# Performance work log

Hardware: AMD Instinct MI355X
Metric: run time of the kernel (lower is better)

The kernel has to match this reference:

```python
import jax, jax.numpy as jnp
import numpy as np
from jax import lax

N, GH, GE, LH, LL = 19, 64, 64, 64, 2
B, T = 256, 256


def _normalized_adjacency(A):
    # A: (..., n, n). Add self-loops, symmetric degree normalization.
    n = A.shape[-1]
    A = A + jnp.eye(n, dtype=A.dtype)
    deg = jnp.clip(A.sum(axis=-1), 1e-6, None)  # (..., n)
    dis = deg ** -0.5
    return A * dis[..., :, None] * dis[..., None, :]


def _graph_encoder(A, w1_w, w1_b, w2_w, w2_b):
    # A: (B, T, n, n) -> (B, T, GE). Node features X = A rows.
    An = _normalized_adjacency(A)
    X = jax.nn.relu(An @ (A @ w1_w.T + w1_b))   # (B,T,n,GH)
    X = jax.nn.relu(An @ (X @ w2_w.T + w2_b))   # (B,T,n,GE)
    return X.mean(axis=-2)


def _lstm_layer(x, Wih, Whh, bih, bhh):
    # x: (B, T, D); PyTorch gate order i,f,g,o. Returns (B, T, H).
    Bb = x.shape[0]
    H = Whh.shape[1]
    xg = x @ Wih.T + (bih + bhh)  # precompute input contributions (B,T,4H)

    def step(carry, xt):
        h, c = carry
        gates = xt + h @ Whh.T
        i, f, g, o = jnp.split(gates, 4, axis=-1)
        c = jax.nn.sigmoid(f) * c + jax.nn.sigmoid(i) * jnp.tanh(g)
        h = jax.nn.sigmoid(o) * jnp.tanh(c)
        return (h, c), h

    h0 = jnp.zeros((Bb, H), x.dtype)
    (_, _), hs = lax.scan(step, (h0, h0), jnp.swapaxes(xg, 0, 1))
    return jnp.swapaxes(hs, 0, 1)


def setup_inputs() -> dict:
    key = jax.random.key(0)
    ks = jax.random.split(key, 20)
    s = 0.1
    inp = {
        'conn': jax.random.uniform(ks[0], (B, T, N, N), jnp.float32),
        'mask': jnp.ones((B, T), jnp.int32),
        'w1_w': jax.random.normal(ks[1], (GH, N), jnp.float32) * s,
        'w1_b': jax.random.normal(ks[2], (GH,), jnp.float32) * s,
        'w2_w': jax.random.normal(ks[3], (GE, GH), jnp.float32) * s,
        'w2_b': jax.random.normal(ks[4], (GE,), jnp.float32) * s,
        'lstm_Wih0': jax.random.normal(ks[5], (4 * LH, GE), jnp.float32) * s,
        'lstm_Whh0': jax.random.normal(ks[6], (4 * LH, LH), jnp.float32) * s,
        'lstm_bih0': jax.random.normal(ks[7], (4 * LH,), jnp.float32) * s,
        'lstm_bhh0': jax.random.normal(ks[8], (4 * LH,), jnp.float32) * s,
        'lstm_Wih1': jax.random.normal(ks[9], (4 * LH, LH), jnp.float32) * s,
        'lstm_Whh1': jax.random.normal(ks[10], (4 * LH, LH), jnp.float32) * s,
        'lstm_bih1': jax.random.normal(ks[11], (4 * LH,), jnp.float32) * s,
        'lstm_bhh1': jax.random.normal(ks[12], (4 * LH,), jnp.float32) * s,
        'fc1_w': jax.random.normal(ks[13], (32, LH), jnp.float32) * s,
        'fc1_b': jax.random.normal(ks[14], (32,), jnp.float32) * s,
        'fc2_w': jax.random.normal(ks[15], (2, 32), jnp.float32) * s,
        'fc2_b': jax.random.normal(ks[16], (2,), jnp.float32) * s,
    }
    return inp


def reference(conn, mask, w1_w, w1_b, w2_w, w2_b,
              lstm_Wih0, lstm_Whh0, lstm_bih0, lstm_bhh0,
              lstm_Wih1, lstm_Whh1, lstm_bih1, lstm_bhh1,
              fc1_w, fc1_b, fc2_w, fc2_b):
    emb = _graph_encoder(conn, w1_w, w1_b, w2_w, w2_b)  # (B,T,GE)
    mf = mask.astype(emb.dtype)
    emb = emb * mf[:, :, None]
    out = _lstm_layer(emb, lstm_Wih0, lstm_Whh0, lstm_bih0, lstm_bhh0)
    out = _lstm_layer(out, lstm_Wih1, lstm_Whh1, lstm_bih1, lstm_bhh1)  # (B,T,LH)
    lengths = jnp.clip(mask.sum(axis=1), 1, None)
    last_idx = jnp.clip(lengths - 1, 0, None)  # (B,)
    last_h = jnp.take_along_axis(out, last_idx[:, None, None], axis=1)[:, 0, :]
    h = jax.nn.relu(last_h @ fc1_w.T + fc1_b)
    return h @ fc2_w.T + fc2_b  # (B,2) logits
```

## Files before the change

kernel.cpp:

```cpp
#include <hip/hip_runtime.h>
#include <hip/hip_bf16.h>
#include <math.h>

#define GN 19
#define BB 256
#define TT 256

typedef short short8 __attribute__((ext_vector_type(8)));
typedef float f4 __attribute__((ext_vector_type(4)));

union Frag { int i[4]; short8 s; };

#define LWAIT() __asm__ volatile("s_waitcnt lgkmcnt(0)" ::: "memory")
#define WGBAR() __asm__ volatile("s_waitcnt lgkmcnt(0)\ns_barrier" ::: "memory")

__device__ __forceinline__ int pkbf(float a, float b) {
    __hip_bfloat162 h2 = __float22bfloat162_rn(make_float2(a, b));
    union { __hip_bfloat162 h; int i; } u; u.h = h2; return u.i;
}

__device__ __forceinline__ float rl(float v, int j) {
    return __int_as_float(__builtin_amdgcn_readlane(__float_as_int(v), j));
}
__device__ __forceinline__ float fexp2(float x) { return __builtin_amdgcn_exp2f(x); }
__device__ __forceinline__ float frcp(float x)  { return __builtin_amdgcn_rcpf(x); }
__device__ __forceinline__ float sigm(float x)  { return frcp(1.f + fexp2(-1.4426950408889634f * x)); }
__device__ __forceinline__ float tanha(float x) { float e = fexp2(2.8853900817779268f * x); return 1.f - 2.f * frcp(e + 1.f); }

__global__ __launch_bounds__(64) void encoder_mfma(
    const float* __restrict__ conn,
    const int*   __restrict__ mask,
    const float* __restrict__ w1_w,
    const float* __restrict__ w1_b,
    const float* __restrict__ w2_w,
    const float* __restrict__ w2_b,
    float* __restrict__ emb,
    int num_graphs)
{
    __shared__ float S[2304];
    __shared__ float dis[32];
    __shared__ float ps[256];

    const int t = threadIdx.x;
    const int l15 = t & 15;
    const int quad = t >> 4;

    float km[8];
    #pragma unroll
    for (int j = 0; j < 8; ++j) km[j] = (quad * 8 + j < GN) ? 1.f : 0.f;

    int rr[6], cc[6];
    #pragma unroll
    for (int i = 0; i < 6; ++i) {
        int e = t + 64 * i;
        rr[i] = e / GN;
        cc[i] = e - rr[i] * GN;
    }

    Frag w1F[4];
    #pragma unroll
    for (int nt = 0; nt < 4; ++nt) {
        int n = nt * 16 + l15;
        #pragma unroll
        for (int p = 0; p < 4; ++p) {
            int k0 = quad * 8 + 2 * p, k1 = k0 + 1;
            float a = (k0 < GN) ? w1_w[n * GN + k0] : 0.f;
            float b = (k1 < GN) ? w1_w[n * GN + k1] : 0.f;
            w1F[nt].i[p] = pkbf(a, b);
        }
    }
    Frag w2F[2][4];
    #pragma unroll
    for (int kt = 0; kt < 2; ++kt)
        #pragma unroll
        for (int nt = 0; nt < 4; ++nt) {
            int n = nt * 16 + l15;
            #pragma unroll
            for (int p = 0; p < 4; ++p) {
                int k = kt * 32 + quad * 8 + 2 * p;
                w2F[kt][nt].i[p] = pkbf(w2_w[n * 64 + k], w2_w[n * 64 + k + 1]);
            }
        }
    float b1v[4], b2v[4];
    #pragma unroll
    for (int nt = 0; nt < 4; ++nt) {
        b1v[nt] = w1_b[nt * 16 + l15];
        b2v[nt] = w2_b[nt * 16 + l15];
    }

    float pf[6];
    {
        int g0 = blockIdx.x < num_graphs ? blockIdx.x : 0;
        const float* Ag = conn + (size_t)g0 * (GN * GN);
        #pragma unroll
        for (int i = 0; i < 6; ++i) {
            int e = t + 64 * i;
            if (e < GN * GN) pf[i] = Ag[e];
        }
    }

    #pragma unroll 1
    for (int g = blockIdx.x; g < num_graphs; g += gridDim.x) {
        #pragma unroll
        for (int i = 0; i < 4; ++i) {
            int s = t + 64 * i;
            int row = s >> 3, c4 = s & 7;
            f4 z = {0.f, 0.f, 0.f, 0.f};
            *(f4*)&S[row * 68 + c4 * 4] = z;
        }
        LWAIT();
        #pragma unroll
        for (int i = 0; i < 6; ++i) {
            if (t + 64 * i < GN * GN) S[rr[i] * 68 + cc[i]] = pf[i];
        }
        {
            int gn = g + gridDim.x;
            const float* Ag = conn + (size_t)(gn < num_graphs ? gn : g) * (GN * GN);
            #pragma unroll
            for (int i = 0; i < 6; ++i) {
                int e = t + 64 * i;
                if (e < GN * GN) pf[i] = Ag[e];
            }
        }
        LWAIT();

        if (t < 32) {
            float dv = 0.f;
            if (t < GN) {
                float d = 1.0f;
                #pragma unroll
                for (int c4 = 0; c4 < 8; ++c4) {
                    f4 v = *(f4*)&S[t * 68 + c4 * 4];
                    d += v.x + v.y + v.z + v.w;
                }
                dv = rsqrtf(d);
            }
            dis[t] = dv;
        }
        LWAIT();

        float dk[8];
        {
            f4 v0 = *(f4*)&dis[quad * 8];
            f4 v1 = *(f4*)&dis[quad * 8 + 4];
            dk[0]=v0.x; dk[1]=v0.y; dk[2]=v0.z; dk[3]=v0.w;
            dk[4]=v1.x; dk[5]=v1.y; dk[6]=v1.z; dk[7]=v1.w;
        }
        Frag aF[2], anF[2];
        #pragma unroll
        for (int mt = 0; mt < 2; ++mt) {
            int m = l15 + 16 * mt;
            float dm = dis[m];
            f4 v0 = *(f4*)&S[m * 68 + quad * 8];
            f4 v1 = *(f4*)&S[m * 68 + quad * 8 + 4];
            float av[8] = {v0.x, v0.y, v0.z, v0.w, v1.x, v1.y, v1.z, v1.w};
            float an[8];
            #pragma unroll
            for (int j = 0; j < 8; ++j) {
                int k = quad * 8 + j;
                an[j] = (av[j] + (m == k ? 1.f : 0.f)) * dm * dk[j];
            }
            #pragma unroll
            for (int p = 0; p < 4; ++p) {
                aF[mt].i[p]  = pkbf(av[2*p], av[2*p+1]);
                anF[mt].i[p] = pkbf(an[2*p], an[2*p+1]);
            }
        }
        LWAIT();

        #pragma unroll
        for (int mt = 0; mt < 2; ++mt)
            #pragma unroll
            for (int nt = 0; nt < 4; ++nt) {
                float bb = b1v[nt];
                f4 c = {bb, bb, bb, bb};
                c = __builtin_amdgcn_mfma_f32_16x16x32_bf16(aF[mt].s, w1F[nt].s, c, 0, 0, 0);
                int col = nt * 16 + l15;
                #pragma unroll
                for (int r = 0; r < 4; ++r)
                    S[col * 36 + (mt * 16 + quad * 4 + r)] = c[r];
            }
        LWAIT();

        Frag hF[4];
        #pragma unroll
        for (int nt = 0; nt < 4; ++nt) {
            int n = nt * 16 + l15;
            f4 v0 = *(f4*)&S[n * 36 + quad * 8];
            f4 v1 = *(f4*)&S[n * 36 + quad * 8 + 4];
            float vv[8] = {v0.x, v0.y, v0.z, v0.w, v1.x, v1.y, v1.z, v1.w};
            #pragma unroll
            for (int p = 0; p < 4; ++p)
                hF[nt].i[p] = pkbf(vv[2*p] * km[2*p], vv[2*p+1] * km[2*p+1]);
        }
        LWAIT();

        #pragma unroll
        for (int mt = 0; mt < 2; ++mt)
            #pragma unroll
            for (int nt = 0; nt < 4; ++nt) {
                f4 c = {0.f, 0.f, 0.f, 0.f};
                c = __builtin_amdgcn_mfma_f32_16x16x32_bf16(anF[mt].s, hF[nt].s, c, 0, 0, 0);
                int col = nt * 16 + l15;
                #pragma unroll
                for (int r = 0; r < 4; ++r)
                    S[(mt * 16 + quad * 4 + r) * 68 + col] = fmaxf(c[r], 0.f);
            }
        LWAIT();

        Frag xF[2][2];
        #pragma unroll
        for (int mt = 0; mt < 2; ++mt) {
            int m = l15 + 16 * mt;
            #pragma unroll
            for (int kt = 0; kt < 2; ++kt) {
                f4 v0 = *(f4*)&S[m * 68 + kt * 32 + quad * 8];
                f4 v1 = *(f4*)&S[m * 68 + kt * 32 + quad * 8 + 4];
                xF[mt][kt].i[0] = pkbf(v0.x, v0.y);
                xF[mt][kt].i[1] = pkbf(v0.z, v0.w);
                xF[mt][kt].i[2] = pkbf(v1.x, v1.y);
                xF[mt][kt].i[3] = pkbf(v1.z, v1.w);
            }
        }
        LWAIT();

        #pragma unroll
        for (int mt = 0; mt < 2; ++mt)
            #pragma unroll
            for (int nt = 0; nt < 4; ++nt) {
                float bb = b2v[nt];
                f4 c = {bb, bb, bb, bb};
                c = __builtin_amdgcn_mfma_f32_16x16x32_bf16(xF[mt][0].s, w2F[0][nt].s, c, 0, 0, 0);
                c = __builtin_amdgcn_mfma_f32_16x16x32_bf16(xF[mt][1].s, w2F[1][nt].s, c, 0, 0, 0);
                int col = nt * 16 + l15;
                #pragma unroll
                for (int r = 0; r < 4; ++r)
                    S[col * 36 + (mt * 16 + quad * 4 + r)] = c[r];
            }
        LWAIT();

        #pragma unroll
        for (int nt = 0; nt < 4; ++nt) {
            int n = nt * 16 + l15;
            f4 v0 = *(f4*)&S[n * 36 + quad * 8];
            f4 v1 = *(f4*)&S[n * 36 + quad * 8 + 4];
            float vv[8] = {v0.x, v0.y, v0.z, v0.w, v1.x, v1.y, v1.z, v1.w};
            #pragma unroll
            for (int p = 0; p < 4; ++p)
                hF[nt].i[p] = pkbf(vv[2*p] * km[2*p], vv[2*p+1] * km[2*p+1]);
        }

        float cs[4];
        #pragma unroll
        for (int nt = 0; nt < 4; ++nt) cs[nt] = 0.f;
        #pragma unroll
        for (int mt = 0; mt < 2; ++mt)
            #pragma unroll
            for (int nt = 0; nt < 4; ++nt) {
                f4 c = {0.f, 0.f, 0.f, 0.f};
                c = __builtin_amdgcn_mfma_f32_16x16x32_bf16(anF[mt].s, hF[nt].s, c, 0, 0, 0);
                if (mt == 0) {
                    cs[nt] += fmaxf(c[0], 0.f) + fmaxf(c[1], 0.f)
                            + fmaxf(c[2], 0.f) + fmaxf(c[3], 0.f);
                } else if (quad == 0) {
                    cs[nt] += fmaxf(c[0], 0.f) + fmaxf(c[1], 0.f) + fmaxf(c[2], 0.f);
                }
            }
        #pragma unroll
        for (int nt = 0; nt < 4; ++nt)
            ps[quad * 64 + nt * 16 + l15] = cs[nt];
        LWAIT();
        float tot = ps[t] + ps[64 + t] + ps[128 + t] + ps[192 + t];
        float mf = (float)mask[g];
        emb[(size_t)g * 64 + t] = tot * (1.f / 19.f) * mf;
        LWAIT();
    }
}

__global__ __launch_bounds__(512, 2) void lstm_fused(
    const float* __restrict__ x,
    const int*   __restrict__ mask,
    const float* __restrict__ Wih0, const float* __restrict__ Whh0,
    const float* __restrict__ bih0, const float* __restrict__ bhh0,
    const float* __restrict__ Wih1, const float* __restrict__ Whh1,
    const float* __restrict__ bih1, const float* __restrict__ bhh1,
    const float* __restrict__ fc1_w, const float* __restrict__ fc1_b,
    const float* __restrict__ fc2_w, const float* __restrict__ fc2_b,
    float* __restrict__ out)
{
    __shared__ float gs0[2][256];
    __shared__ float gs1[2][256];
    __shared__ float h0buf[2][64];
    __shared__ float hd[32];
    __shared__ int li_s;

    const int tid = threadIdx.x;
    const int grp = tid >> 8;
    const int r   = tid & 255;
    const int l   = tid & 63;
    const int b   = blockIdx.x;

    const float* __restrict__ Wih = grp ? Wih1 : Wih0;
    const float* __restrict__ Whh = grp ? Whh1 : Whh0;
    float wi[64], wh[64];
    {
        const float4* p = (const float4*)(Wih + r * 64);
        const float4* q = (const float4*)(Whh + r * 64);
        #pragma unroll
        for (int j = 0; j < 16; ++j) {
            ((float4*)wi)[j] = p[j];
            ((float4*)wh)[j] = q[j];
        }
    }
    const float bias = grp ? (bih1[r] + bhh1[r]) : (bih0[r] + bhh0[r]);

    if (tid < 256) gs0[0][tid] = (float)mask[b * TT + tid];
    __syncthreads();
    if (tid == 0) {
        float s = 0.f;
        for (int t = 0; t < TT; ++t) s += gs0[0][t];
        int li = (int)s - 1;
        li = li < 0 ? 0 : (li > TT - 1 ? TT - 1 : li);
        li_s = li;
    }
    __syncthreads();
    const int lastidx = li_s;

    const float* __restrict__ xb = x + (size_t)b * TT * 64;
    float (*gsL)[256] = grp ? gs1 : gs0;

    float h = 0.f, c = 0.f, xc = 0.f, hl = 0.f;

    if (grp == 0) {
        float n0 = 0.f, n1 = 0.f, n2 = 0.f, n3 = 0.f;
        #pragma unroll
        for (int j = 0; j < 64; j += 4) {
            n0 = fmaf(xb[j],     wi[j],     n0);
            n1 = fmaf(xb[j + 1], wi[j + 1], n1);
            n2 = fmaf(xb[j + 2], wi[j + 2], n2);
            n3 = fmaf(xb[j + 3], wi[j + 3], n3);
        }
        xc = (n0 + n1) + (n2 + n3);
    }

    #pragma unroll 1
    for (int it = 0; it < TT + 2; ++it) {
        const int p = it & 1;

        f4 xr[16];
        if (grp == 0) {
            int tn = it + 1; if (tn > TT - 1) tn = TT - 1;
            const f4* __restrict__ ern = (const f4*)(xb + (size_t)tn * 64);
            #pragma unroll
            for (int k = 0; k < 16; ++k) xr[k] = ern[k];

            if (it < TT) {
                float a0 = bias + xc, a1 = 0.f, a2 = 0.f, a3 = 0.f;
                #pragma unroll
                for (int j = 0; j < 64; j += 4) {
                    a0 = fmaf(rl(h, j),     wh[j],     a0);
                    a1 = fmaf(rl(h, j + 1), wh[j + 1], a1);
                    a2 = fmaf(rl(h, j + 2), wh[j + 2], a2);
                    a3 = fmaf(rl(h, j + 3), wh[j + 3], a3);
                }
                gs0[p][r] = (a0 + a1) + (a2 + a3);
            }
        } else {
            if (it >= 2) {
                float a0 = bias + xc, a1 = 0.f, a2 = 0.f, a3 = 0.f;
                #pragma unroll
                for (int j = 0; j < 64; j += 4) {
                    a0 = fmaf(rl(h, j),     wh[j],     a0);
                    a1 = fmaf(rl(h, j + 1), wh[j + 1], a1);
                    a2 = fmaf(rl(h, j + 2), wh[j + 2], a2);
                    a3 = fmaf(rl(h, j + 3), wh[j + 3], a3);
                }
                gs1[p][r] = (a0 + a1) + (a2 + a3);
            }
        }

        WGBAR();

        if (grp == 0) {
            if (it < TT) {
                const float* gp = gs0[p];
                float gi = gp[l], gf = gp[64 + l], gg = gp[128 + l], go = gp[192 + l];
                c = sigm(gf) * c + sigm(gi) * tanha(gg);
                h = sigm(go) * tanha(c);
                if (tid < 64) h0buf[p][l] = h;
            }
            float n0 = 0.f, n1 = 0.f, n2 = 0.f, n3 = 0.f;
            #pragma unroll
            for (int k = 0; k < 16; ++k) {
                f4 v = xr[k];
                n0 = fmaf(v.x, wi[4*k],     n0);
                n1 = fmaf(v.y, wi[4*k + 1], n1);
                n2 = fmaf(v.z, wi[4*k + 2], n2);
                n3 = fmaf(v.w, wi[4*k + 3], n3);
            }
            xc = (n0 + n1) + (n2 + n3);
        } else {
            if (it >= 2) {
                const float* gp = gs1[p];
                float gi = gp[l], gf = gp[64 + l], gg = gp[128 + l], go = gp[192 + l];
                c = sigm(gf) * c + sigm(gi) * tanha(gg);
                h = sigm(go) * tanha(c);
                if (it - 2 == lastidx) hl = h;
            }
            if (it >= 1 && it <= TT) {
                const f4* __restrict__ hp = (const f4*)h0buf[p ^ 1];
                float n0 = 0.f, n1 = 0.f, n2 = 0.f, n3 = 0.f;
                #pragma unroll
                for (int k = 0; k < 16; ++k) {
                    f4 v = hp[k];
                    n0 = fmaf(v.x, wi[4*k],     n0);
                    n1 = fmaf(v.y, wi[4*k + 1], n1);
                    n2 = fmaf(v.z, wi[4*k + 2], n2);
                    n3 = fmaf(v.w, wi[4*k + 3], n3);
                }
                xc = (n0 + n1) + (n2 + n3);
            }
        }
    }

    if (grp == 1 && r < 64) {
        if (l < 32) {
            float acc = fc1_b[l];
            const float* fw = fc1_w + l * 64;
            #pragma unroll
            for (int j = 0; j < 64; ++j)
                acc = fmaf(fw[j], rl(hl, j), acc);
            hd[l] = fmaxf(acc, 0.f);
        }
        LWAIT();
        if (l < 2) {
            float acc = fc2_b[l];
            #pragma unroll
            for (int j = 0; j < 32; ++j)
                acc = fmaf(fc2_w[l * 32 + j], hd[j], acc);
            out[b * 2 + l] = acc;
        }
    }
}

extern "C" void kernel_launch(void* const* d_in, const int* in_sizes, int n_in,
                              void* d_out, int out_size, void* d_ws, size_t ws_size,
                              hipStream_t stream)
{
    const float* conn  = (const float*)d_in[0];
    const int*   mask  = (const int*)  d_in[1];
    const float* w1_w  = (const float*)d_in[2];
    const float* w1_b  = (const float*)d_in[3];
    const float* w2_w  = (const float*)d_in[4];
    const float* w2_b  = (const float*)d_in[5];
    const float* Wih0  = (const float*)d_in[6];
    const float* Whh0  = (const float*)d_in[7];
    const float* bih0  = (const float*)d_in[8];
    const float* bhh0  = (const float*)d_in[9];
    const float* Wih1  = (const float*)d_in[10];
    const float* Whh1  = (const float*)d_in[11];
    const float* bih1  = (const float*)d_in[12];
    const float* bhh1  = (const float*)d_in[13];
    const float* fc1_w = (const float*)d_in[14];
    const float* fc1_b = (const float*)d_in[15];
    const float* fc2_w = (const float*)d_in[16];
    const float* fc2_b = (const float*)d_in[17];

    float* out = (float*)d_out;
    float* emb = (float*)d_ws;

    const int num_graphs = BB * TT;

    encoder_mfma<<<8192, 64, 0, stream>>>(
        conn, mask, w1_w, w1_b, w2_w, w2_b, emb, num_graphs);

    lstm_fused<<<BB, 512, 0, stream>>>(
        emb, mask, Wih0, Whh0, bih0, bhh0, Wih1, Whh1, bih1, bhh1,
        fc1_w, fc1_b, fc2_w, fc2_b, out);
}
```

Before: 617.4 us.

## Batch 16 sequences per block and compute LSTM gates with bf16 MFMA

The LSTM kernel is rewritten so each block handles 16 sequences and computes both layers' gate matmuls with bf16 MFMA instructions. Gate rows are interleaved so each lane's accumulator holds the i,f,g,o values for one unit. Hidden states are split into high and low bf16 halves to keep close to fp32 accuracy, and both layers run in the same step with layer 1 lagging by one timestep. The aim is to replace the per-thread scalar FMA dot products over 256 blocks with matrix-core work. The cost is only 16 blocks on the GPU, which leaves most compute units idle, plus extra MFMAs for the split precision.

```diff
diff --git a/kernel.cpp b/kernel.cpp
--- a/kernel.cpp
+++ b/kernel.cpp
@@ -13,15 +13,14 @@
 
 #define LWAIT() __asm__ volatile("s_waitcnt lgkmcnt(0)" ::: "memory")
 #define WGBAR() __asm__ volatile("s_waitcnt lgkmcnt(0)\ns_barrier" ::: "memory")
+
+#define MFMA(a,b,c) __builtin_amdgcn_mfma_f32_16x16x32_bf16(a,b,c,0,0,0)
 
 __device__ __forceinline__ int pkbf(float a, float b) {
     __hip_bfloat162 h2 = __float22bfloat162_rn(make_float2(a, b));
     union { __hip_bfloat162 h; int i; } u; u.h = h2; return u.i;
 }
 
-__device__ __forceinline__ float rl(float v, int j) {
-    return __int_as_float(__builtin_amdgcn_readlane(__float_as_int(v), j));
-}
 __device__ __forceinline__ float fexp2(float x) { return __builtin_amdgcn_exp2f(x); }
 __device__ __forceinline__ float frcp(float x)  { return __builtin_amdgcn_rcpf(x); }
 __device__ __forceinline__ float sigm(float x)  { return frcp(1.f + fexp2(-1.4426950408889634f * x)); }
@@ -174,7 +173,7 @@
             for (int nt = 0; nt < 4; ++nt) {
                 float bb = b1v[nt];
                 f4 c = {bb, bb, bb, bb};
-                c = __builtin_amdgcn_mfma_f32_16x16x32_bf16(aF[mt].s, w1F[nt].s, c, 0, 0, 0);
+                c = MFMA(aF[mt].s, w1F[nt].s, c);
                 int col = nt * 16 + l15;
                 #pragma unroll
                 for (int r = 0; r < 4; ++r)
@@ -200,7 +199,7 @@
             #pragma unroll
             for (int nt = 0; nt < 4; ++nt) {
                 f4 c = {0.f, 0.f, 0.f, 0.f};
-                c = __builtin_amdgcn_mfma_f32_16x16x32_bf16(anF[mt].s, hF[nt].s, c, 0, 0, 0);
+                c = MFMA(anF[mt].s, hF[nt].s, c);
                 int col = nt * 16 + l15;
                 #pragma unroll
                 for (int r = 0; r < 4; ++r)
@@ -230,8 +229,8 @@
             for (int nt = 0; nt < 4; ++nt) {
                 float bb = b2v[nt];
                 f4 c = {bb, bb, bb, bb};
-                c = __builtin_amdgcn_mfma_f32_16x16x32_bf16(xF[mt][0].s, w2F[0][nt].s, c, 0, 0, 0);
-                c = __builtin_amdgcn_mfma_f32_16x16x32_bf16(xF[mt][1].s, w2F[1][nt].s, c, 0, 0, 0);
+                c = MFMA(xF[mt][0].s, w2F[0][nt].s, c);
+                c = MFMA(xF[mt][1].s, w2F[1][nt].s, c);
                 int col = nt * 16 + l15;
                 #pragma unroll
                 for (int r = 0; r < 4; ++r)
@@ -239,6 +238,7 @@
             }
         LWAIT();
 
+        Frag hG[4];
         #pragma unroll
         for (int nt = 0; nt < 4; ++nt) {
             int n = nt * 16 + l15;
@@ -247,7 +247,7 @@
             float vv[8] = {v0.x, v0.y, v0.z, v0.w, v1.x, v1.y, v1.z, v1.w};
             #pragma unroll
             for (int p = 0; p < 4; ++p)
-                hF[nt].i[p] = pkbf(vv[2*p] * km[2*p], vv[2*p+1] * km[2*p+1]);
+                hG[nt].i[p] = pkbf(vv[2*p] * km[2*p], vv[2*p+1] * km[2*p+1]);
         }
 
         float cs[4];
@@ -258,7 +258,7 @@
             #pragma unroll
             for (int nt = 0; nt < 4; ++nt) {
                 f4 c = {0.f, 0.f, 0.f, 0.f};
-                c = __builtin_amdgcn_mfma_f32_16x16x32_bf16(anF[mt].s, hF[nt].s, c, 0, 0, 0);
+                c = MFMA(anF[mt].s, hG[nt].s, c);
                 if (mt == 0) {
                     cs[nt] += fmaxf(c[0], 0.f) + fmaxf(c[1], 0.f)
                             + fmaxf(c[2], 0.f) + fmaxf(c[3], 0.f);
@@ -277,7 +277,7 @@
     }
 }
 
-__global__ __launch_bounds__(512, 2) void lstm_fused(
+__global__ __launch_bounds__(512, 2) void lstm_mfma(
     const float* __restrict__ x,
     const int*   __restrict__ mask,
     const float* __restrict__ Wih0, const float* __restrict__ Whh0,
@@ -288,158 +288,223 @@
     const float* __restrict__ fc2_w, const float* __restrict__ fc2_b,
     float* __restrict__ out)
 {
-    __shared__ float gs0[2][256];
-    __shared__ float gs1[2][256];
-    __shared__ float h0buf[2][64];
-    __shared__ float hd[32];
-    __shared__ int li_s;
-
-    const int tid = threadIdx.x;
-    const int grp = tid >> 8;
-    const int r   = tid & 255;
-    const int l   = tid & 63;
-    const int b   = blockIdx.x;
-
-    const float* __restrict__ Wih = grp ? Wih1 : Wih0;
-    const float* __restrict__ Whh = grp ? Whh1 : Whh0;
-    float wi[64], wh[64];
+    __shared__ int   h0b[2][16 * 68];
+    __shared__ int   h1b[2][16 * 68];
+    __shared__ float hlast[16][68];
+    __shared__ float red[512];
+    __shared__ int   li_s[16];
+
+    const int tid  = threadIdx.x;
+    const int w    = tid >> 6;
+    const int lane = tid & 63;
+    const int l15  = lane & 15;
+    const int quad = lane >> 4;
+    const int bb0  = blockIdx.x * 16;
+
     {
-        const float4* p = (const float4*)(Wih + r * 64);
-        const float4* q = (const float4*)(Whh + r * 64);
-        #pragma unroll
-        for (int j = 0; j < 16; ++j) {
-            ((float4*)wi)[j] = p[j];
-            ((float4*)wh)[j] = q[j];
-        }
-    }
-    const float bias = grp ? (bih1[r] + bhh1[r]) : (bih0[r] + bhh0[r]);
-
-    if (tid < 256) gs0[0][tid] = (float)mask[b * TT + tid];
+        int b16 = tid >> 5, j = tid & 31;
+        int s = 0;
+        #pragma unroll
+        for (int c8 = 0; c8 < 8; ++c8)
+            s += mask[(bb0 + b16) * TT + j + 32 * c8];
+        red[tid] = (float)s;
+    }
     __syncthreads();
-    if (tid == 0) {
+    if (tid < 16) {
         float s = 0.f;
-        for (int t = 0; t < TT; ++t) s += gs0[0][t];
+        #pragma unroll
+        for (int j = 0; j < 32; ++j) s += red[tid * 32 + j];
         int li = (int)s - 1;
-        li = li < 0 ? 0 : (li > TT - 1 ? TT - 1 : li);
-        li_s = li;
+        li_s[tid] = li < 0 ? 0 : (li > TT - 1 ? TT - 1 : li);
     }
     __syncthreads();
-    const int lastidx = li_s;
-
-    const float* __restrict__ xb = x + (size_t)b * TT * 64;
-    float (*gsL)[256] = grp ? gs1 : gs0;
-
-    float h = 0.f, c = 0.f, xc = 0.f, hl = 0.f;
-
-    if (grp == 0) {
-        float n0 = 0.f, n1 = 0.f, n2 = 0.f, n3 = 0.f;
-        #pragma unroll
-        for (int j = 0; j < 64; j += 4) {
-            n0 = fmaf(xb[j],     wi[j],     n0);
-            n1 = fmaf(xb[j + 1], wi[j + 1], n1);
-            n2 = fmaf(xb[j + 2], wi[j + 2], n2);
-            n3 = fmaf(xb[j + 3], wi[j + 3], n3);
-        }
-        xc = (n0 + n1) + (n2 + n3);
+    const int li = li_s[l15];
+
+    Frag Aih0[2][2], Ahh0[2][2], Aih1[2][2], Ahh1[2][2];
+    f4 bias0v[2], bias1v[2];
+    #pragma unroll
+    for (int mt = 0; mt < 2; ++mt) {
+        int mg = 2 * w + mt;
+        int orig = (l15 & 3) * 64 + (mg * 4 + (l15 >> 2));
+        #pragma unroll
+        for (int kt = 0; kt < 2; ++kt)
+            #pragma unroll
+            for (int p = 0; p < 4; ++p) {
+                int k = kt * 32 + quad * 8 + 2 * p;
+                Aih0[mt][kt].i[p] = pkbf(Wih0[orig * 64 + k], Wih0[orig * 64 + k + 1]);
+                Ahh0[mt][kt].i[p] = pkbf(Whh0[orig * 64 + k], Whh0[orig * 64 + k + 1]);
+                Aih1[mt][kt].i[p] = pkbf(Wih1[orig * 64 + k], Wih1[orig * 64 + k + 1]);
+                Ahh1[mt][kt].i[p] = pkbf(Whh1[orig * 64 + k], Whh1[orig * 64 + k + 1]);
+            }
+        int uu = mg * 4 + quad;
+        #pragma unroll
+        for (int r = 0; r < 4; ++r) {
+            bias0v[mt][r] = bih0[r * 64 + uu] + bhh0[r * 64 + uu];
+            bias1v[mt][r] = bih1[r * 64 + uu] + bhh1[r * 64 + uu];
+        }
+    }
+    const int uoff0 = (2 * w + 0) * 4 + quad;
+    const int uoff1 = (2 * w + 1) * 4 + quad;
+
+    Frag BX[2], BH0h[2], BH0l[2], BH1h[2], BH1l[2];
+    #pragma unroll
+    for (int kt = 0; kt < 2; ++kt)
+        #pragma unroll
+        for (int p = 0; p < 4; ++p) {
+            BX[kt].i[p] = 0; BH0h[kt].i[p] = 0; BH0l[kt].i[p] = 0;
+            BH1h[kt].i[p] = 0; BH1l[kt].i[p] = 0;
+        }
+    float c0s[2] = {0.f, 0.f}, c1s[2] = {0.f, 0.f}, h1last[2] = {0.f, 0.f};
+
+    const float* __restrict__ xb = x + (size_t)(bb0 + l15) * TT * 64;
+    f4 xpre[4];
+    {
+        const f4* p0 = (const f4*)(xb + quad * 8);
+        const f4* p1 = (const f4*)(xb + 32 + quad * 8);
+        xpre[0] = p0[0]; xpre[1] = p0[1];
+        xpre[2] = p1[0]; xpre[3] = p1[1];
     }
 
     #pragma unroll 1
-    for (int it = 0; it < TT + 2; ++it) {
-        const int p = it & 1;
-
-        f4 xr[16];
-        if (grp == 0) {
-            int tn = it + 1; if (tn > TT - 1) tn = TT - 1;
-            const f4* __restrict__ ern = (const f4*)(xb + (size_t)tn * 64);
-            #pragma unroll
-            for (int k = 0; k < 16; ++k) xr[k] = ern[k];
-
-            if (it < TT) {
-                float a0 = bias + xc, a1 = 0.f, a2 = 0.f, a3 = 0.f;
+    for (int it = 0; it <= TT; ++it) {
+        const int cur = it & 1;
+
+        if (it < TT) {
+            #pragma unroll
+            for (int kt = 0; kt < 2; ++kt) {
+                f4 v0 = xpre[kt * 2], v1 = xpre[kt * 2 + 1];
+                BX[kt].i[0] = pkbf(v0.x, v0.y);
+                BX[kt].i[1] = pkbf(v0.z, v0.w);
+                BX[kt].i[2] = pkbf(v1.x, v1.y);
+                BX[kt].i[3] = pkbf(v1.z, v1.w);
+            }
+            int tn = it + 1 < TT ? it + 1 : TT - 1;
+            const f4* p0 = (const f4*)(xb + (size_t)tn * 64 + quad * 8);
+            const f4* p1 = (const f4*)(xb + (size_t)tn * 64 + 32 + quad * 8);
+            xpre[0] = p0[0]; xpre[1] = p0[1];
+            xpre[2] = p1[0]; xpre[3] = p1[1];
+        }
+
+        f4 g0[2], g1[2];
+        if (it < TT) {
+            #pragma unroll
+            for (int mt = 0; mt < 2; ++mt) {
+                f4 c = bias0v[mt];
+                c = MFMA(Aih0[mt][0].s, BX[0].s,   c);
+                c = MFMA(Aih0[mt][1].s, BX[1].s,   c);
+                c = MFMA(Ahh0[mt][0].s, BH0h[0].s, c);
+                c = MFMA(Ahh0[mt][1].s, BH0h[1].s, c);
+                c = MFMA(Ahh0[mt][0].s, BH0l[0].s, c);
+                c = MFMA(Ahh0[mt][1].s, BH0l[1].s, c);
+                g0[mt] = c;
+            }
+        }
+        if (it >= 1) {
+            #pragma unroll
+            for (int mt = 0; mt < 2; ++mt) {
+                f4 c = bias1v[mt];
+                c = MFMA(Aih1[mt][0].s, BH0h[0].s, c);
+                c = MFMA(Aih1[mt][1].s, BH0h[1].s, c);
+                c = MFMA(Aih1[mt][0].s, BH0l[0].s, c);
+                c = MFMA(Aih1[mt][1].s, BH0l[1].s, c);
+                c = MFMA(Ahh1[mt][0].s, BH1h[0].s, c);
+                c = MFMA(Ahh1[mt][1].s, BH1h[1].s, c);
+                c = MFMA(Ahh1[mt][0].s, BH1l[0].s, c);
+                c = MFMA(Ahh1[mt][1].s, BH1l[1].s, c);
+                g1[mt] = c;
+            }
+        }
+
+        if (it < TT) {
+            #pragma unroll
+            for (int mt = 0; mt < 2; ++mt) {
+                f4 g = g0[mt];
+                float si = sigm(g[0]), sf = sigm(g[1]);
+                float tg = tanha(g[2]), so = sigm(g[3]);
+                float cc = fmaf(sf, c0s[mt], si * tg);
+                c0s[mt] = cc;
+                float h = so * tanha(cc);
+                unsigned hb = __float_as_uint(h);
+                float hhi = __uint_as_float(hb & 0xFFFF0000u);
+                float hlo = h - hhi;
+                unsigned lopk = (unsigned)pkbf(hlo, hlo);
+                int packed = (int)__builtin_amdgcn_perm(lopk, hb, 0x05040302u);
+                h0b[cur][l15 * 68 + (mt ? uoff1 : uoff0)] = packed;
+            }
+        }
+        if (it >= 1) {
+            #pragma unroll
+            for (int mt = 0; mt < 2; ++mt) {
+                f4 g = g1[mt];
+                float si = sigm(g[0]), sf = sigm(g[1]);
+                float tg = tanha(g[2]), so = sigm(g[3]);
+                float cc = fmaf(sf, c1s[mt], si * tg);
+                c1s[mt] = cc;
+                float h = so * tanha(cc);
+                if (it - 1 == li) h1last[mt] = h;
+                unsigned hb = __float_as_uint(h);
+                float hhi = __uint_as_float(hb & 0xFFFF0000u);
+                float hlo = h - hhi;
+                unsigned lopk = (unsigned)pkbf(hlo, hlo);
+                int packed = (int)__builtin_amdgcn_perm(lopk, hb, 0x05040302u);
+                h1b[cur][l15 * 68 + (mt ? uoff1 : uoff0)] = packed;
+            }
+        }
+
+        WGBAR();
+
+        if (it < TT) {
+            #pragma unroll
+            for (int kt = 0; kt < 2; ++kt) {
+                const int4* pp = (const int4*)&h0b[cur][l15 * 68 + kt * 32 + quad * 8];
+                int4 va = pp[0], vb = pp[1];
+                BH0h[kt].i[0] = (int)__builtin_amdgcn_perm((unsigned)va.y, (unsigned)va.x, 0x05040100u);
+                BH0h[kt].i[1] = (int)__builtin_amdgcn_perm((unsigned)va.w, (unsigned)va.z, 0x05040100u);
+                BH0h[kt].i[2] = (int)__builtin_amdgcn_perm((unsigned)vb.y, (unsigned)vb.x, 0x05040100u);
+                BH0h[kt].i[3] = (int)__builtin_amdgcn_perm((unsigned)vb.w, (unsigned)vb.z, 0x05040100u);
+                BH0l[kt].i[0] = (int)__builtin_amdgcn_perm((unsigned)va.y, (unsigned)va.x, 0x07060302u);
+                BH0l[kt].i[1] = (int)__builtin_amdgcn_perm((unsigned)va.w, (unsigned)va.z, 0x07060302u);
+                BH0l[kt].i[2] = (int)__builtin_amdgcn_perm((unsigned)vb.y, (unsigned)vb.x, 0x07060302u);
+                BH0l[kt].i[3] = (int)__builtin_amdgcn_perm((unsigned)vb.w, (unsigned)vb.z, 0x07060302u);
+            }
+            if (it >= 1) {
                 #pragma unroll
-                for (int j = 0; j < 64; j += 4) {
-                    a0 = fmaf(rl(h, j),     wh[j],     a0);
-                    a1 = fmaf(rl(h, j + 1), wh[j + 1], a1);
-                    a2 = fmaf(rl(h, j + 2), wh[j + 2], a2);
-                    a3 = fmaf(rl(h, j + 3), wh[j + 3], a3);
+                for (int kt = 0; kt < 2; ++kt) {
+                    const int4* pp = (const int4*)&h1b[cur][l15 * 68 + kt * 32 + quad * 8];
+                    int4 va = pp[0], vb = pp[1];
+                    BH1h[kt].i[0] = (int)__builtin_amdgcn_perm((unsigned)va.y, (unsigned)va.x, 0x05040100u);
+                    BH1h[kt].i[1] = (int)__builtin_amdgcn_perm((unsigned)va.w, (unsigned)va.z, 0x05040100u);
+                    BH1h[kt].i[2] = (int)__builtin_amdgcn_perm((unsigned)vb.y, (unsigned)vb.x, 0x05040100u);
+                    BH1h[kt].i[3] = (int)__builtin_amdgcn_perm((unsigned)vb.w, (unsigned)vb.z, 0x05040100u);
+                    BH1l[kt].i[0] = (int)__builtin_amdgcn_perm((unsigned)va.y, (unsigned)va.x, 0x07060302u);
+                    BH1l[kt].i[1] = (int)__builtin_amdgcn_perm((unsigned)va.w, (unsigned)va.z, 0x07060302u);
+                    BH1l[kt].i[2] = (int)__builtin_amdgcn_perm((unsigned)vb.y, (unsigned)vb.x, 0x07060302u);
+                    BH1l[kt].i[3] = (int)__builtin_amdgcn_perm((unsigned)vb.w, (unsigned)vb.z, 0x07060302u);
                 }
-                gs0[p][r] = (a0 + a1) + (a2 + a3);
-            }
-        } else {
-            if (it >= 2) {
-                float a0 = bias + xc, a1 = 0.f, a2 = 0.f, a3 = 0.f;
-                #pragma unroll
-                for (int j = 0; j < 64; j += 4) {
-                    a0 = fmaf(rl(h, j),     wh[j],     a0);
-                    a1 = fmaf(rl(h, j + 1), wh[j + 1], a1);
-                    a2 = fmaf(rl(h, j + 2), wh[j + 2], a2);
-                    a3 = fmaf(rl(h, j + 3), wh[j + 3], a3);
-                }
-                gs1[p][r] = (a0 + a1) + (a2 + a3);
-            }
-        }
-
-        WGBAR();
-
-        if (grp == 0) {
-            if (it < TT) {
-                const float* gp = gs0[p];
-                float gi = gp[l], gf = gp[64 + l], gg = gp[128 + l], go = gp[192 + l];
-                c = sigm(gf) * c + sigm(gi) * tanha(gg);
-                h = sigm(go) * tanha(c);
-                if (tid < 64) h0buf[p][l] = h;
-            }
-            float n0 = 0.f, n1 = 0.f, n2 = 0.f, n3 = 0.f;
-            #pragma unroll
-            for (int k = 0; k < 16; ++k) {
-                f4 v = xr[k];
-                n0 = fmaf(v.x, wi[4*k],     n0);
-                n1 = fmaf(v.y, wi[4*k + 1], n1);
-                n2 = fmaf(v.z, wi[4*k + 2], n2);
-                n3 = fmaf(v.w, wi[4*k + 3], n3);
-            }
-            xc = (n0 + n1) + (n2 + n3);
-        } else {
-            if (it >= 2) {
-                const float* gp = gs1[p];
-                float gi = gp[l], gf = gp[64 + l], gg = gp[128 + l], go = gp[192 + l];
-                c = sigm(gf) * c + sigm(gi) * tanha(gg);
-                h = sigm(go) * tanha(c);
-                if (it - 2 == lastidx) hl = h;
-            }
-            if (it >= 1 && it <= TT) {
-                const f4* __restrict__ hp = (const f4*)h0buf[p ^ 1];
-                float n0 = 0.f, n1 = 0.f, n2 = 0.f, n3 = 0.f;
-                #pragma unroll
-                for (int k = 0; k < 16; ++k) {
-                    f4 v = hp[k];
-                    n0 = fmaf(v.x, wi[4*k],     n0);
-                    n1 = fmaf(v.y, wi[4*k + 1], n1);
-                    n2 = fmaf(v.z, wi[4*k + 2], n2);
-                    n3 = fmaf(v.w, wi[4*k + 3], n3);
-                }
-                xc = (n0 + n1) + (n2 + n3);
-            }
-        }
-    }
-
-    if (grp == 1 && r < 64) {
-        if (l < 32) {
-            float acc = fc1_b[l];
-            const float* fw = fc1_w + l * 64;
-            #pragma unroll
-            for (int j = 0; j < 64; ++j)
-                acc = fmaf(fw[j], rl(hl, j), acc);
-            hd[l] = fmaxf(acc, 0.f);
-        }
-        LWAIT();
-        if (l < 2) {
-            float acc = fc2_b[l];
-            #pragma unroll
-            for (int j = 0; j < 32; ++j)
-                acc = fmaf(fc2_w[l * 32 + j], hd[j], acc);
-            out[b * 2 + l] = acc;
-        }
+            }
+        }
+    }
+
+    hlast[l15][uoff0] = h1last[0];
+    hlast[l15][uoff1] = h1last[1];
+    __syncthreads();
+    {
+        int b = tid >> 5, o = tid & 31;
+        float acc = fc1_b[o];
+        const float* fw = fc1_w + o * 64;
+        #pragma unroll
+        for (int j = 0; j < 64; ++j)
+            acc = fmaf(hlast[b][j], fw[j], acc);
+        red[b * 32 + o] = fmaxf(acc, 0.f);
+    }
+    __syncthreads();
+    if (tid < 32) {
+        int b = tid >> 1, o = tid & 1;
+        float acc = fc2_b[o];
+        #pragma unroll
+        for (int j = 0; j < 32; ++j)
+            acc = fmaf(fc2_w[o * 32 + j], red[b * 32 + j], acc);
+        out[(bb0 + b) * 2 + o] = acc;
     }
 }
 
@@ -474,7 +539,7 @@
     encoder_mfma<<<8192, 64, 0, stream>>>(
         conn, mask, w1_w, w1_b, w2_w, w2_b, emb, num_graphs);
 
-    lstm_fused<<<BB, 512, 0, stream>>>(
+    lstm_mfma<<<16, 512, 0, stream>>>(
         emb, mask, Wih0, Whh0, bih0, bhh0, Wih1, Whh1, bih1, bhh1,
         fc1_w, fc1_b, fc2_w, fc2_b, out);
 }
```

Result: no change. 615.2 us (-0.4%).
